# Optimization experiments

Measured on AMD Instinct MI355X. Metric: run time of the kernel, lower is better.

## Reference

```python
import jax, jax.numpy as jnp
import numpy as np

B = 16384        # batch size
D = 128          # embedding dim == ln_bot[-1]
N_EMB = 26       # number of sparse tables
VOCAB = 50000    # rows per table
LN_BOT = [13, 512, 256, 128]
LN_TOP = [479, 1024, 1024, 512, 1]
# triangular indices matching: li=[i for i in range(ni) for j in range(i)] (offset=0, no self-interaction)
LI, LJ = np.tril_indices(N_EMB + 1, -1)


def _init_linear(key, n_in, n_out):
    kw, kb = jax.random.split(key)
    lim = 1.0 / np.sqrt(n_in)
    W = jax.random.uniform(kw, (n_in, n_out), minval=-lim, maxval=lim, dtype=jnp.float32)
    b = jax.random.uniform(kb, (n_out,), minval=-lim, maxval=lim, dtype=jnp.float32)
    return W, b


def setup_inputs() -> dict:
    key = jax.random.key(0)
    ks = jax.random.split(key, 3 + len(LN_BOT) - 1 + len(LN_TOP) - 1)
    inp = {
        "dense_x": jax.random.normal(ks[0], (B, LN_BOT[0]), dtype=jnp.float32),
        "indices": jax.random.randint(ks[1], (N_EMB, B), 0, VOCAB),
        "emb_tables": jax.random.normal(ks[2], (N_EMB, VOCAB, D), dtype=jnp.float32) * 0.01,
    }
    k = 3
    for i in range(len(LN_BOT) - 1):
        W, b = _init_linear(ks[k], LN_BOT[i], LN_BOT[i + 1]); k += 1
        inp[f"bot_W{i}"], inp[f"bot_b{i}"] = W, b
    for i in range(len(LN_TOP) - 1):
        W, b = _init_linear(ks[k], LN_TOP[i], LN_TOP[i + 1]); k += 1
        inp[f"top_W{i}"], inp[f"top_b{i}"] = W, b
    return inp


def reference(dense_x, indices, emb_tables,
              bot_W0, bot_b0, bot_W1, bot_b1, bot_W2, bot_b2,
              top_W0, top_b0, top_W1, top_b1, top_W2, top_b2, top_W3, top_b3):
    # bottom MLP (sigmoid_bot=-1 -> all ReLU)
    x = dense_x
    for W, b in ((bot_W0, bot_b0), (bot_W1, bot_b1), (bot_W2, bot_b2)):
        x = jax.nn.relu(x @ W + b)                      # [B, 128]

    # embedding lookups (bag size 1 per table)
    emb = jax.vmap(lambda t, i: t[i])(emb_tables, indices)   # [26, B, D]
    emb = jnp.transpose(emb, (1, 0, 2))                      # [B, 26, D]

    # dot interaction
    T = jnp.concatenate([x[:, None, :], emb], axis=1)        # [B, 27, D]
    Z = jnp.einsum('bid,bjd->bij', T, T)                     # [B, 27, 27]
    Zflat = Z[:, LI, LJ]                                     # [B, 351]
    R = jnp.concatenate([x, Zflat], axis=1)                  # [B, 479]

    # top MLP (sigmoid on last layer, sigmoid_top=3)
    h = R
    for W, b in ((top_W0, top_b0), (top_W1, top_b1), (top_W2, top_b2)):
        h = jax.nn.relu(h @ W + b)
    p = jax.nn.sigmoid(h @ top_W3 + top_b3)                  # [B, 1]
    return jnp.clip(p, 0.0, 1.0)                             # loss_threshold = 0.0
```

## Files before the change

### kernel.cpp

```cpp
#include <hip/hip_runtime.h>

typedef __attribute__((ext_vector_type(8))) short short8;
typedef __attribute__((ext_vector_type(4))) float f32x4;
typedef __attribute__((ext_vector_type(16))) float f32x16;

#define B_ROWS 16384

__device__ __forceinline__ float bf2f(ushort u){ return __uint_as_float(((uint)u)<<16); }
__device__ __forceinline__ ushort f2bf(float f){
  uint u = __float_as_uint(f);
  u = u + 0x7FFFu + ((u>>16)&1u);
  return (ushort)(u>>16);
}
__device__ __forceinline__ void gload_lds16(const void* g, void* l){
  __builtin_amdgcn_global_load_lds((const __attribute__((address_space(1))) unsigned*)g,
                                   (__attribute__((address_space(3))) unsigned*)l, 16, 0, 0);
}

struct TArgs { const float* in; ushort* out; int K, N, Kp; };
struct PrepArgs {
  const float* x; const float* W0; const float* b0; ushort* act0;
  TArgs t[5];
  float* partial;
};

__global__ __launch_bounds__(256) void prep(PrepArgs a)
{
  const int idx = blockIdx.x;
  const int tid = threadIdx.x;
  __shared__ float tile[32][33];

  if (idx < 32768){
    int i = idx*256 + tid;
    int b = i>>9, n = i&511;
    const float* xr = a.x + (size_t)b*13;
    float s = a.b0[n];
    #pragma unroll
    for (int k=0;k<13;k++) s += xr[k]*a.W0[k*512+n];
    a.act0[i] = f2bf(fmaxf(s,0.f));
    return;
  }
  if (idx >= 34976){
    a.partial[(idx-34976)*256 + tid] = 0.f;
    return;
  }
  int t = idx - 32768, s, kx, ny;
  if (t < 128)              { s=0; kx=t&15; ny=t>>4; }
  else if ((t-=128) < 32)   { s=1; kx=t&7 ; ny=t>>3; }
  else if ((t-=32) < 512)   { s=2; kx=t&15; ny=t>>4; }
  else if ((t-=512) < 1024) { s=3; kx=t&31; ny=t>>5; }
  else { t-=1024;             s=4; kx=t&31; ny=t>>5; }
  TArgs ta = a.t[s];
  int k0 = kx*32, n0 = ny*32;
  const int c = tid & 31, r8 = tid >> 5;
  #pragma unroll
  for (int p=0;p<4;p++){
    int k = k0 + r8 + p*8;
    tile[r8+p*8][c] = (k < ta.K) ? ta.in[(size_t)k*ta.N + n0 + c] : 0.f;
  }
  __syncthreads();
  #pragma unroll
  for (int p=0;p<4;p++){
    int n = n0 + r8 + p*8;
    ta.out[(size_t)n*ta.Kp + k0 + c] = f2bf(tile[c][r8+p*8]);
  }
}

__global__ __launch_bounds__(256) void bot12(const ushort* __restrict__ act0,
    const ushort* __restrict__ W1t, const float* __restrict__ b1,
    const ushort* __restrict__ W2t, const float* __restrict__ b2,
    ushort* __restrict__ R)
{
  __shared__ __align__(16) char smem[147456];
  const int tid = threadIdx.x;
  const int wave = tid>>6, lane = tid&63;
  const int lr = lane&15, lg = lane>>4;
  const int bm = blockIdx.x*64;

  #pragma unroll
  for (int j=0;j<16;j++){
    uint lin = (uint)tid*16u + (uint)j*4096u;
    gload_lds16((const char*)W2t + (lin ^ (((lin>>9)&7u)<<4)), smem + 81920 + lin);
  }

  auto stage = [&](int buf, int kt){
    #pragma unroll
    for (int c=0;c<2;c++){
      uint lin = (uint)tid*16u + (uint)c*4096u;
      uint row = lin>>7, scol = (lin&127u) ^ (((lin>>7)&7u)<<4);
      gload_lds16((const char*)act0 + (((size_t)(bm+row)*512 + (uint)kt*64u)<<1) + scol,
                  smem + (buf?8192:0) + lin);
    }
    #pragma unroll
    for (int c=0;c<8;c++){
      uint lin = (uint)tid*16u + (uint)c*4096u;
      uint row = lin>>7, scol = (lin&127u) ^ (((lin>>7)&7u)<<4);
      gload_lds16((const char*)W1t + (((size_t)row*512 + (uint)kt*64u)<<1) + scol,
                  smem + 16384 + (buf?32768:0) + lin);
    }
  };

  f32x4 acc[4][4];
  #pragma unroll
  for (int m=0;m<4;m++)
    #pragma unroll
    for (int n=0;n<4;n++)
      #pragma unroll
      for (int j=0;j<4;j++) acc[m][n][j] = 0.f;

  stage(0,0);
  int cur = 0;
  for (int t=0;t<8;t++){
    int nx = (t+1<8) ? t+1 : 0;
    stage(cur^1, nx);
    asm volatile("s_waitcnt vmcnt(10)" ::: "memory");
    __builtin_amdgcn_s_barrier();
    asm volatile("" ::: "memory");
    const char* lAc = smem + (cur?8192:0);
    const char* lBc = smem + 16384 + (cur?32768:0);
    #pragma unroll
    for (int kk2=0;kk2<2;kk2++){
      short8 af[4], bfr[4];
      #pragma unroll
      for (int m=0;m<4;m++){
        uint row = (uint)(m*16+lr);
        uint l = row*128u + (uint)kk2*64u + (uint)lg*16u;
        af[m] = *(const short8*)(lAc + (l ^ ((row&7u)<<4)));
      }
      #pragma unroll
      for (int n=0;n<4;n++){
        uint row = (uint)(wave*64 + n*16+lr);
        uint l = row*128u + (uint)kk2*64u + (uint)lg*16u;
        bfr[n] = *(const short8*)(lBc + (l ^ ((row&7u)<<4)));
      }
      #pragma unroll
      for (int m=0;m<4;m++)
        #pragma unroll
        for (int n=0;n<4;n++)
          acc[m][n] = __builtin_amdgcn_mfma_f32_16x16x32_bf16(af[m], bfr[n], acc[m][n], 0,0,0);
    }
    asm volatile("" ::: "memory");
    __builtin_amdgcn_s_barrier();
    cur ^= 1;
  }
  asm volatile("s_waitcnt vmcnt(0)" ::: "memory");
  __syncthreads();

  ushort* a1 = (ushort*)smem;
  #pragma unroll
  for (int n=0;n<4;n++){
    int col = wave*64 + n*16 + lr;
    float bv = b1[col];
    #pragma unroll
    for (int m=0;m<4;m++)
      #pragma unroll
      for (int j=0;j<4;j++){
        int row = m*16 + lg*4 + j;
        a1[(uint)row*264u + (uint)col] = f2bf(fmaxf(acc[m][n][j] + bv, 0.f));
      }
  }
  __syncthreads();

  f32x4 acc2[4][2];
  #pragma unroll
  for (int m=0;m<4;m++)
    #pragma unroll
    for (int n=0;n<2;n++)
      #pragma unroll
      for (int j=0;j<4;j++) acc2[m][n][j] = 0.f;

  const char* w2c = smem + 81920;
  #pragma unroll
  for (int ks=0;ks<8;ks++){
    short8 af[4], bw[2];
    #pragma unroll
    for (int m=0;m<4;m++)
      af[m] = *(const short8*)&a1[(uint)(m*16+lr)*264u + (uint)ks*32u + (uint)lg*8u];
    #pragma unroll
    for (int n=0;n<2;n++){
      uint row = (uint)(wave*32 + n*16 + lr);
      uint l = row*512u + (uint)ks*64u + (uint)lg*16u;
      bw[n] = *(const short8*)(w2c + (l ^ ((row&7u)<<4)));
    }
    #pragma unroll
    for (int m=0;m<4;m++)
      #pragma unroll
      for (int n=0;n<2;n++)
        acc2[m][n] = __builtin_amdgcn_mfma_f32_16x16x32_bf16(af[m], bw[n], acc2[m][n], 0,0,0);
  }

  #pragma unroll
  for (int n=0;n<2;n++){
    int col = wave*32 + n*16 + lr;
    float bv = b2[col];
    #pragma unroll
    for (int m=0;m<4;m++)
      #pragma unroll
      for (int j=0;j<4;j++){
        int row = bm + m*16 + lg*4 + j;
        R[(size_t)row*512 + col] = f2bf(fmaxf(acc2[m][n][j] + bv, 0.f));
      }
  }
}

template<int BN, bool FUSE>
__global__ __launch_bounds__(512, 2) void gemm256(const ushort* __restrict__ A,
    const ushort* __restrict__ Bt, const float* __restrict__ bias,
    ushort* __restrict__ C, int K, int ldc,
    const float* __restrict__ w3, float* __restrict__ partial)
{
  constexpr int  NF = BN/128;
  constexpr int  LB = BN/128;
  constexpr uint BR = (uint)BN*32u;
  constexpr uint BUFSZ = 16384u + 2u*BR;
  __shared__ __align__(16) ushort lds[2*BUFSZ];

  const int tid = threadIdx.x;
  const int wave = tid>>6, lane = tid&63;
  const uint wm = (uint)(wave>>2), wn = (uint)(wave&3);
  const uint lc = (uint)(lane&31), hi = (uint)(lane>>5);
  const int bm = blockIdx.x*256, bn = blockIdx.y*BN;
  const int nt = K>>6, niter = nt>>1;

  f32x16 acc[4][NF];
  #pragma unroll
  for (int m=0;m<4;m++)
    #pragma unroll
    for (int n=0;n<NF;n++)
      #pragma unroll
      for (int j=0;j<16;j++) acc[m][n][j] = 0.f;

  short8 bfr[2][NF];

#define STAGE(MAT, KH, TILE, SBUF) do{                                          \
    int kt_ = (TILE);                                                           \
    int ktc_ = (kt_ < nt) ? kt_ : 0;                                            \
    const ushort* gb_ = (MAT) ? Bt : A;                                         \
    const uint ro_ = (MAT) ? (uint)bn : (uint)bm;                               \
    const uint rb_ = (uint)(SBUF)*BUFSZ + ((MAT) ? (16384u + (uint)(KH)*BR)     \
                                                 : ((uint)(KH)*8192u));         \
    const int nl_ = (MAT) ? LB : 2;                                             \
    _Pragma("unroll")                                                           \
    for (int j_=0; j_<nl_; ++j_){                                               \
      uint lin_ = (uint)tid*16u + (uint)j_*8192u;                               \
      uint src_ = lin_ ^ (((lin_>>7)&3u)<<4);                                   \
      uint row_ = src_>>6, colb_ = src_&63u;                                    \
      const char* g_ = (const char*)gb_ +                                       \
        (((size_t)(ro_+row_)*(size_t)K + (size_t)ktc_*64 + (KH)*32)<<1) + colb_;\
      gload_lds16(g_, (char*)lds + (size_t)rb_*2 + lin_);                       \
    }                                                                           \
  }while(0)

#define PHASE(CBUF, KKH, MH, BLOAD, SMAT, SKH, STILE, SBUF, CKPT) do{           \
    const uint ab_ = (uint)(CBUF)*BUFSZ + (uint)(KKH)*8192u;                    \
    short8 af_[2][2];                                                           \
    _Pragma("unroll")                                                           \
    for (int mfl_=0; mfl_<2; ++mfl_){                                           \
      uint r_ = wm*128u + ((uint)(MH)*2u+(uint)mfl_)*32u + lc;                  \
      _Pragma("unroll")                                                         \
      for (int k2_=0; k2_<2; ++k2_){                                            \
        uint l_ = r_*64u + hi*16u + (uint)k2_*32u;                              \
        af_[mfl_][k2_] = *(const short8*)((const char*)lds + (size_t)ab_*2      \
                                   + (l_ ^ (((l_>>7)&3u)<<4)));                 \
      }                                                                         \
    }                                                                           \
    if (BLOAD){                                                                 \
      const uint bb_ = (uint)(CBUF)*BUFSZ + 16384u + (uint)(KKH)*BR;            \
      _Pragma("unroll")                                                         \
      for (int nf_=0; nf_<NF; ++nf_){                                           \
        uint r_ = wn*(uint)(BN/4) + (uint)nf_*32u + lc;                         \
        _Pragma("unroll")                                                       \
        for (int k2_=0; k2_<2; ++k2_){                                          \
          uint l_ = r_*64u + hi*16u + (uint)k2_*32u;                            \
          bfr[k2_][nf_] = *(const short8*)((const char*)lds + (size_t)bb_*2     \
                                     + (l_ ^ (((l_>>7)&3u)<<4)));               \
        }                                                                       \
      }                                                                         \
    }                                                                           \
    STAGE(SMAT, SKH, STILE, SBUF);                                              \
    asm volatile("" ::: "memory");                                              \
    __builtin_amdgcn_s_barrier();                                               \
    asm volatile("" ::: "memory");                                              \
    __builtin_amdgcn_s_setprio(1);                                              \
    _Pragma("unroll")                                                           \
    for (int mfl_=0; mfl_<2; ++mfl_)                                            \
      _Pragma("unroll")                                                         \
      for (int nf_=0; nf_<NF; ++nf_)                                            \
        _Pragma("unroll")                                                       \
        for (int k2_=0; k2_<2; ++k2_)                                           \
          acc[(MH)*2+mfl_][nf_] = __builtin_amdgcn_mfma_f32_32x32x16_bf16(      \
              af_[mfl_][k2_], bfr[k2_][nf_], acc[(MH)*2+mfl_][nf_], 0,0,0);     \
    __builtin_amdgcn_s_setprio(0);                                              \
    if (CKPT){                                                                  \
      if constexpr (LB==2) asm volatile("s_waitcnt vmcnt(8)" ::: "memory");     \
      else                 asm volatile("s_waitcnt vmcnt(6)" ::: "memory");     \
    }                                                                           \
    asm volatile("" ::: "memory");                                              \
    __builtin_amdgcn_s_barrier();                                               \
  }while(0)

  STAGE(0,0,0,0); STAGE(1,0,0,0); STAGE(0,1,0,0); STAGE(1,1,0,0);
  STAGE(0,0,1,1); STAGE(1,0,1,1);
  if constexpr (LB==2) asm volatile("s_waitcnt vmcnt(4)" ::: "memory");
  else                 asm volatile("s_waitcnt vmcnt(3)" ::: "memory");
  asm volatile("" ::: "memory");
  __builtin_amdgcn_s_barrier();

  for (int i=0; i<niter; ++i){
    const int O  = 2*i+1;
    const int E2 = 2*i+2;
    const int O2 = 2*i+3;
    PHASE(0,0,0,true , 0,1,O ,1, false);
    PHASE(0,0,1,false, 1,1,O ,1, true );
    PHASE(0,1,0,true , 0,0,E2,0, false);
    PHASE(0,1,1,false, 1,0,E2,0, true );
    PHASE(1,0,0,true , 0,1,E2,0, false);
    PHASE(1,0,1,false, 1,1,E2,0, true );
    PHASE(1,1,0,true , 0,0,O2,1, false);
    PHASE(1,1,1,false, 1,0,O2,1, true );
  }
#undef PHASE
#undef STAGE

  if constexpr (FUSE){
    int col = bn + (int)wn*(BN/4) + (int)lc;
    float bv = bias[col];
    float wv = w3[col];
    #pragma unroll
    for (int mf=0; mf<4; ++mf){
      #pragma unroll
      for (int reg=0; reg<16; ++reg){
        float v = fmaxf(acc[mf][0][reg] + bv, 0.f) * wv;
        #pragma unroll
        for (int off=1; off<32; off<<=1) v += __shfl_xor(v, off);
        if (lc == 0){
          int row = bm + (int)wm*128 + mf*32 + (reg&3) + 8*(reg>>2) + 4*(int)hi;
          atomicAdd(&partial[row], v);
        }
      }
    }
  } else {
    #pragma unroll
    for (int nf=0; nf<NF; ++nf){
      int col = bn + (int)wn*(BN/4) + nf*32 + (int)lc;
      float bv = bias[col];
      #pragma unroll
      for (int mf=0; mf<4; ++mf){
        #pragma unroll
        for (int reg=0; reg<16; ++reg){
          int row = bm + (int)wm*128 + mf*32 + (reg&3) + 8*(reg>>2) + 4*(int)hi;
          float v = acc[mf][nf][reg] + bv;
          C[(size_t)row*ldc + col] = f2bf(fmaxf(v, 0.f));
        }
      }
    }
  }
}

__global__ __launch_bounds__(256) void interact(const int* __restrict__ idx,
    const float* __restrict__ emb, ushort* __restrict__ R)
{
  __shared__ __align__(16) ushort Tl[4][32][136];
  const int w = threadIdx.x>>6, l = threadIdx.x&63;
  const int b = blockIdx.x*4 + w;
  ushort* Rrow = R + (size_t)b*512;

  uint xv = ((const uint*)Rrow)[l];
  *(uint*)&Tl[w][0][2*l] = xv;

  int myidx = (l<26) ? idx[(size_t)l*B_ROWS + b] : 0;
  const int half = l>>5, lc = l&31;
  #pragma unroll
  for (int i=0;i<13;i++){
    const int row = 2*i + 1 + half;
    int e = __shfl(myidx, row - 1);
    const float4* rp = (const float4*)(emb + ((size_t)(row-1)*50000 + (size_t)e)*128);
    float4 v = rp[lc];
    uint2 pk;
    pk.x = (uint)f2bf(v.x) | ((uint)f2bf(v.y)<<16);
    pk.y = (uint)f2bf(v.z) | ((uint)f2bf(v.w)<<16);
    *(uint2*)&Tl[w][row][4*lc] = pk;
  }
  __syncthreads();

  f32x16 acc;
  #pragma unroll
  for (int i=0;i<16;i++) acc[i] = 0.f;
  #pragma unroll
  for (int kk=0;kk<8;kk++){
    short8 fa = *(const short8*)((const char*)&Tl[w][0][0] + (size_t)(l&31)*272 + kk*32 + (l>>5)*16);
    acc = __builtin_amdgcn_mfma_f32_32x32x16_bf16(fa, fa, acc, 0,0,0);
  }

  const int c = l&31;
  #pragma unroll
  for (int j=0;j<16;j++){
    int r = (j&3) + 8*(j>>2) + 4*(l>>5);
    if (c < r && r <= 26) Rrow[128 + r*(r-1)/2 + c] = f2bf(acc[j]);
  }
  if (l < 33) Rrow[479 + l] = 0;
}

__global__ __launch_bounds__(256) void sigm(const float* __restrict__ partial,
    const float* __restrict__ b3, float* __restrict__ out)
{
  int i = blockIdx.x*256 + threadIdx.x;
  float h = partial[i] + b3[0];
  float p = 1.f/(1.f + expf(-h));
  out[i] = fminf(fmaxf(p, 0.f), 1.f);
}

extern "C" void kernel_launch(void* const* d_in, const int* in_sizes, int n_in,
                              void* d_out, int out_size, void* d_ws, size_t ws_size,
                              hipStream_t stream)
{
  const float* dense_x = (const float*)d_in[0];
  const int*   indices = (const int*)d_in[1];
  const float* emb     = (const float*)d_in[2];
  const float* bW0 = (const float*)d_in[3];  const float* bb0 = (const float*)d_in[4];
  const float* bW1 = (const float*)d_in[5];  const float* bb1 = (const float*)d_in[6];
  const float* bW2 = (const float*)d_in[7];  const float* bb2 = (const float*)d_in[8];
  const float* tW0 = (const float*)d_in[9];  const float* tb0 = (const float*)d_in[10];
  const float* tW1 = (const float*)d_in[11]; const float* tb1 = (const float*)d_in[12];
  const float* tW2 = (const float*)d_in[13]; const float* tb2 = (const float*)d_in[14];
  const float* tW3 = (const float*)d_in[15]; const float* tb3 = (const float*)d_in[16];
  float* out = (float*)d_out;
  const int Bn = B_ROWS;

  char* ws = (char*)d_ws;
  size_t o = 0;
  auto alloc = [&](size_t bytes)->char*{ char* r = ws + o; o += (bytes + 255) & ~(size_t)255; return r; };
  ushort* wtB1 = (ushort*)alloc(256*512*2);
  ushort* wtB2 = (ushort*)alloc(128*256*2);
  ushort* wtT0 = (ushort*)alloc(1024*512*2);
  ushort* wtT1 = (ushort*)alloc((size_t)1024*1024*2);
  ushort* wtT2 = (ushort*)alloc(512*1024*2);
  float*  partial = (float*)alloc(B_ROWS*4);
  ushort* P    = (ushort*)alloc((size_t)Bn*512*2);
  ushort* h1   = (ushort*)alloc((size_t)Bn*1024*2);
  ushort* h2   = (ushort*)alloc((size_t)Bn*1024*2);
  (void)ws_size; (void)in_sizes; (void)n_in; (void)out_size;

  PrepArgs pa;
  pa.x = dense_x; pa.W0 = bW0; pa.b0 = bb0; pa.act0 = P;
  pa.t[0] = { bW1, wtB1, 512 , 256 , 512  };
  pa.t[1] = { bW2, wtB2, 256 , 128 , 256  };
  pa.t[2] = { tW0, wtT0, 479 , 1024, 512  };
  pa.t[3] = { tW1, wtT1, 1024, 1024, 1024 };
  pa.t[4] = { tW2, wtT2, 1024, 512 , 1024 };
  pa.partial = partial;
  prep<<<35040,256,0,stream>>>(pa);

  bot12<<<256,256,0,stream>>>(P, wtB1, bb1, wtB2, bb2, P);

  interact<<<Bn/4,256,0,stream>>>(indices, emb, P);

  gemm256<256,false><<<dim3(64,4),512,0,stream>>>(P,  wtT0, tb0, h1, 512 , 1024, nullptr, nullptr);
  gemm256<256,false><<<dim3(64,4),512,0,stream>>>(h1, wtT1, tb1, h2, 1024, 1024, nullptr, nullptr);
  gemm256<128,true ><<<dim3(64,4),512,0,stream>>>(h2, wtT2, tb2, nullptr, 1024, 0, tW3, partial);
  sigm<<<Bn/256,256,0,stream>>>(partial, tb3, out);
}
```

Before: 184.4 us.

## Fuse sigmoid into last GEMM via atomic counter; halve bot12 tile rows

The final sigmoid kernel is removed. The last fused GEMM now counts finished column-blocks per row-block with an atomic counter, and the last block to arrive applies bias, sigmoid and clamp over that row tile. The counter sits right after the partial buffer and is zeroed by an extra prep block. Separately, bot12 now processes 32 rows per block instead of 64 with a smaller LDS footprint, which doubles its grid and reads W2 straight from global memory instead of staging it in LDS. This aims to cut one launch and raise occupancy in the bottom MLP, at the cost of an extra fence and atomic in the GEMM epilogue and more global reads of W2.

```diff
diff --git a/kernel.cpp b/kernel.cpp
--- a/kernel.cpp
+++ b/kernel.cpp
@@ -41,7 +41,8 @@
     return;
   }
   if (idx >= 34976){
-    a.partial[(idx-34976)*256 + tid] = 0.f;
+    int j = (idx-34976)*256 + tid;
+    if (j < 16448) a.partial[j] = 0.f;
     return;
   }
   int t = idx - 32768, s, kx, ny;
@@ -71,38 +72,31 @@
     const ushort* __restrict__ W2t, const float* __restrict__ b2,
     ushort* __restrict__ R)
 {
-  __shared__ __align__(16) char smem[147456];
+  __shared__ __align__(16) char smem[73728];
   const int tid = threadIdx.x;
   const int wave = tid>>6, lane = tid&63;
   const int lr = lane&15, lg = lane>>4;
-  const int bm = blockIdx.x*64;
-
-  #pragma unroll
-  for (int j=0;j<16;j++){
-    uint lin = (uint)tid*16u + (uint)j*4096u;
-    gload_lds16((const char*)W2t + (lin ^ (((lin>>9)&7u)<<4)), smem + 81920 + lin);
-  }
+  const int bm = blockIdx.x*32;
 
   auto stage = [&](int buf, int kt){
-    #pragma unroll
-    for (int c=0;c<2;c++){
-      uint lin = (uint)tid*16u + (uint)c*4096u;
-      uint row = lin>>7, scol = (lin&127u) ^ (((lin>>7)&7u)<<4);
+    {
+      uint lin = (uint)tid*16u;
+      uint row = lin>>7, scol = (lin&127u) ^ ((row&7u)<<4);
       gload_lds16((const char*)act0 + (((size_t)(bm+row)*512 + (uint)kt*64u)<<1) + scol,
-                  smem + (buf?8192:0) + lin);
+                  smem + (buf?4096:0) + lin);
     }
     #pragma unroll
     for (int c=0;c<8;c++){
       uint lin = (uint)tid*16u + (uint)c*4096u;
-      uint row = lin>>7, scol = (lin&127u) ^ (((lin>>7)&7u)<<4);
+      uint row = lin>>7, scol = (lin&127u) ^ ((row&7u)<<4);
       gload_lds16((const char*)W1t + (((size_t)row*512 + (uint)kt*64u)<<1) + scol,
-                  smem + 16384 + (buf?32768:0) + lin);
+                  smem + 8192 + (buf?32768:0) + lin);
     }
   };
 
-  f32x4 acc[4][4];
-  #pragma unroll
-  for (int m=0;m<4;m++)
+  f32x4 acc[2][4];
+  #pragma unroll
+  for (int m=0;m<2;m++)
     #pragma unroll
     for (int n=0;n<4;n++)
       #pragma unroll
@@ -111,18 +105,17 @@
   stage(0,0);
   int cur = 0;
   for (int t=0;t<8;t++){
-    int nx = (t+1<8) ? t+1 : 0;
-    stage(cur^1, nx);
-    asm volatile("s_waitcnt vmcnt(10)" ::: "memory");
+    stage(cur^1, (t+1<8) ? t+1 : 0);
+    asm volatile("s_waitcnt vmcnt(9)" ::: "memory");
     __builtin_amdgcn_s_barrier();
     asm volatile("" ::: "memory");
-    const char* lAc = smem + (cur?8192:0);
-    const char* lBc = smem + 16384 + (cur?32768:0);
+    const char* lAc = smem + (cur?4096:0);
+    const char* lBc = smem + 8192 + (cur?32768:0);
     #pragma unroll
     for (int kk2=0;kk2<2;kk2++){
-      short8 af[4], bfr[4];
-      #pragma unroll
-      for (int m=0;m<4;m++){
+      short8 af[2], bfr[4];
+      #pragma unroll
+      for (int m=0;m<2;m++){
         uint row = (uint)(m*16+lr);
         uint l = row*128u + (uint)kk2*64u + (uint)lg*16u;
         af[m] = *(const short8*)(lAc + (l ^ ((row&7u)<<4)));
@@ -134,7 +127,7 @@
         bfr[n] = *(const short8*)(lBc + (l ^ ((row&7u)<<4)));
       }
       #pragma unroll
-      for (int m=0;m<4;m++)
+      for (int m=0;m<2;m++)
         #pragma unroll
         for (int n=0;n<4;n++)
           acc[m][n] = __builtin_amdgcn_mfma_f32_16x16x32_bf16(af[m], bfr[n], acc[m][n], 0,0,0);
@@ -152,7 +145,7 @@
     int col = wave*64 + n*16 + lr;
     float bv = b1[col];
     #pragma unroll
-    for (int m=0;m<4;m++)
+    for (int m=0;m<2;m++)
       #pragma unroll
       for (int j=0;j<4;j++){
         int row = m*16 + lg*4 + j;
@@ -161,29 +154,27 @@
   }
   __syncthreads();
 
-  f32x4 acc2[4][2];
-  #pragma unroll
-  for (int m=0;m<4;m++)
+  f32x4 acc2[2][2];
+  #pragma unroll
+  for (int m=0;m<2;m++)
     #pragma unroll
     for (int n=0;n<2;n++)
       #pragma unroll
       for (int j=0;j<4;j++) acc2[m][n][j] = 0.f;
 
-  const char* w2c = smem + 81920;
   #pragma unroll
   for (int ks=0;ks<8;ks++){
-    short8 af[4], bw[2];
-    #pragma unroll
-    for (int m=0;m<4;m++)
+    short8 af[2], bw[2];
+    #pragma unroll
+    for (int m=0;m<2;m++)
       af[m] = *(const short8*)&a1[(uint)(m*16+lr)*264u + (uint)ks*32u + (uint)lg*8u];
     #pragma unroll
     for (int n=0;n<2;n++){
-      uint row = (uint)(wave*32 + n*16 + lr);
-      uint l = row*512u + (uint)ks*64u + (uint)lg*16u;
-      bw[n] = *(const short8*)(w2c + (l ^ ((row&7u)<<4)));
-    }
-    #pragma unroll
-    for (int m=0;m<4;m++)
+      int row = wave*32 + n*16 + lr;
+      bw[n] = *(const short8*)(W2t + (size_t)row*256 + ks*32 + lg*8);
+    }
+    #pragma unroll
+    for (int m=0;m<2;m++)
       #pragma unroll
       for (int n=0;n<2;n++)
         acc2[m][n] = __builtin_amdgcn_mfma_f32_16x16x32_bf16(af[m], bw[n], acc2[m][n], 0,0,0);
@@ -194,7 +185,7 @@
     int col = wave*32 + n*16 + lr;
     float bv = b2[col];
     #pragma unroll
-    for (int m=0;m<4;m++)
+    for (int m=0;m<2;m++)
       #pragma unroll
       for (int j=0;j<4;j++){
         int row = bm + m*16 + lg*4 + j;
@@ -207,7 +198,8 @@
 __global__ __launch_bounds__(512, 2) void gemm256(const ushort* __restrict__ A,
     const ushort* __restrict__ Bt, const float* __restrict__ bias,
     ushort* __restrict__ C, int K, int ldc,
-    const float* __restrict__ w3, float* __restrict__ partial)
+    const float* __restrict__ w3, float* __restrict__ partial,
+    int* __restrict__ cnt, const float* __restrict__ b3, float* __restrict__ outp)
 {
   constexpr int  NF = BN/128;
   constexpr int  LB = BN/128;
@@ -339,6 +331,21 @@
         }
       }
     }
+    __threadfence();
+    volatile int* flag = (volatile int*)lds;
+    if (tid == 0){
+      int old = atomicAdd(cnt + blockIdx.x, 1);
+      *flag = (old == 3) ? 1 : 0;
+    }
+    __syncthreads();
+    if (*flag){
+      float bb = b3[0];
+      for (int r = tid; r < 256; r += 512){
+        float h = atomicAdd(&partial[bm + r], 0.f) + bb;
+        float p = 1.f/(1.f + expf(-h));
+        outp[bm + r] = fminf(fmaxf(p, 0.f), 1.f);
+      }
+    }
   } else {
     #pragma unroll
     for (int nf=0; nf<NF; ++nf){
@@ -399,15 +406,6 @@
     if (c < r && r <= 26) Rrow[128 + r*(r-1)/2 + c] = f2bf(acc[j]);
   }
   if (l < 33) Rrow[479 + l] = 0;
-}
-
-__global__ __launch_bounds__(256) void sigm(const float* __restrict__ partial,
-    const float* __restrict__ b3, float* __restrict__ out)
-{
-  int i = blockIdx.x*256 + threadIdx.x;
-  float h = partial[i] + b3[0];
-  float p = 1.f/(1.f + expf(-h));
-  out[i] = fminf(fmaxf(p, 0.f), 1.f);
 }
 
 extern "C" void kernel_launch(void* const* d_in, const int* in_sizes, int n_in,
@@ -435,10 +433,11 @@
   ushort* wtT0 = (ushort*)alloc(1024*512*2);
   ushort* wtT1 = (ushort*)alloc((size_t)1024*1024*2);
   ushort* wtT2 = (ushort*)alloc(512*1024*2);
-  float*  partial = (float*)alloc(B_ROWS*4);
+  float*  partial = (float*)alloc((B_ROWS+64)*4);
   ushort* P    = (ushort*)alloc((size_t)Bn*512*2);
   ushort* h1   = (ushort*)alloc((size_t)Bn*1024*2);
   ushort* h2   = (ushort*)alloc((size_t)Bn*1024*2);
+  int* cnt = (int*)(partial + B_ROWS);
   (void)ws_size; (void)in_sizes; (void)n_in; (void)out_size;
 
   PrepArgs pa;
@@ -449,14 +448,16 @@
   pa.t[3] = { tW1, wtT1, 1024, 1024, 1024 };
   pa.t[4] = { tW2, wtT2, 1024, 512 , 1024 };
   pa.partial = partial;
-  prep<<<35040,256,0,stream>>>(pa);
-
-  bot12<<<256,256,0,stream>>>(P, wtB1, bb1, wtB2, bb2, P);
+  prep<<<35041,256,0,stream>>>(pa);
+
+  bot12<<<512,256,0,stream>>>(P, wtB1, bb1, wtB2, bb2, P);
 
   interact<<<Bn/4,256,0,stream>>>(indices, emb, P);
 
-  gemm256<256,false><<<dim3(64,4),512,0,stream>>>(P,  wtT0, tb0, h1, 512 , 1024, nullptr, nullptr);
-  gemm256<256,false><<<dim3(64,4),512,0,stream>>>(h1, wtT1, tb1, h2, 1024, 1024, nullptr, nullptr);
-  gemm256<128,true ><<<dim3(64,4),512,0,stream>>>(h2, wtT2, tb2, nullptr, 1024, 0, tW3, partial);
-  sigm<<<Bn/256,256,0,stream>>>(partial, tb3, out);
-}
+  gemm256<256,false><<<dim3(64,4),512,0,stream>>>(P,  wtT0, tb0, h1, 512 , 1024,
+                                                  nullptr, nullptr, nullptr, nullptr, nullptr);
+  gemm256<256,false><<<dim3(64,4),512,0,stream>>>(h1, wtT1, tb1, h2, 1024, 1024,
+                                                  nullptr, nullptr, nullptr, nullptr, nullptr);
+  gemm256<128,true ><<<dim3(64,4),512,0,stream>>>(h2, wtT2, tb2, nullptr, 1024, 0,
+                                                  tW3, partial, cnt, tb3, out);
+}
```

Measured after the change: 213.1 us. 1.16x slower.
